# Performance work log

Measured on AMD Instinct MI355X. Metric: run time of the kernel, lower is better.

Reference implementation:

```python
import jax, jax.numpy as jnp
import numpy as np

DIM, H, KVH = 1024, 16, 4
HD = DIM // H            # head_dim = 64
KV_DIM = KVH * HD        # 256
ROPE_BASE = 10000.0
EPS = 1e-6


def setup_inputs() -> dict:
    key = jax.random.key(0)
    ks = jax.random.split(key, 6)
    B, S = 4, 2048
    x = jax.random.normal(ks[0], (B, S, DIM), dtype=jnp.float32)
    sc = 0.02
    Wq = jax.random.normal(ks[1], (DIM, DIM), dtype=jnp.float32) * sc
    Wk = jax.random.normal(ks[2], (KV_DIM, DIM), dtype=jnp.float32) * sc
    Wv = jax.random.normal(ks[3], (KV_DIM, DIM), dtype=jnp.float32) * sc
    Wo = jax.random.normal(ks[4], (DIM, DIM), dtype=jnp.float32) * sc
    q_gain = jnp.full((H,), 1.5, dtype=jnp.float32)
    return {"x": x, "Wq": Wq, "Wk": Wk, "Wv": Wv, "Wo": Wo, "q_gain": q_gain}


def _rms_norm(t):
    return t * jax.lax.rsqrt(jnp.mean(t * t, axis=-1, keepdims=True) + EPS)


def _rotary(seqlen, dtype):
    inv_freq = 1.0 / (ROPE_BASE ** (jnp.arange(0, HD, 2, dtype=jnp.float32) / HD))
    t = jnp.arange(seqlen, dtype=jnp.float32)
    freqs = jnp.outer(t, inv_freq)                      # [S, HD/2]
    return jnp.cos(freqs).astype(dtype)[None, None], jnp.sin(freqs).astype(dtype)[None, None]


def _apply_rot(t, cos, sin):
    half = t.shape[-1] // 2
    t1, t2 = t[..., :half], t[..., half:]
    return jnp.concatenate((t1 * cos + t2 * sin, -t1 * sin + t2 * cos), axis=-1)


def reference(x, Wq, Wk, Wv, Wo, q_gain):
    B, S, D = x.shape
    q = (x @ Wq.T).reshape(B, S, H, HD).transpose(0, 2, 1, 3)      # [B,H,S,HD]
    k = (x @ Wk.T).reshape(B, S, KVH, HD).transpose(0, 2, 1, 3)    # [B,KVH,S,HD]
    v = (x @ Wv.T).reshape(B, S, KVH, HD).transpose(0, 2, 1, 3)
    q, k = _rms_norm(q), _rms_norm(k)
    cos, sin = _rotary(S, q.dtype)
    q, k = _apply_rot(q, cos, sin), _apply_rot(k, cos, sin)
    q = q * q_gain.astype(q.dtype)[None, :, None, None]
    rep = H // KVH
    k_exp = jnp.repeat(k, rep, axis=1)                              # GQA expand
    v_exp = jnp.repeat(v, rep, axis=1)
    scores = jnp.einsum('bhqd,bhkd->bhqk', q, k_exp) / np.sqrt(HD)
    causal = jnp.tril(jnp.ones((S, S), dtype=bool))
    scores = jnp.where(causal[None, None], scores, jnp.finfo(scores.dtype).min)
    attn = jax.nn.softmax(scores, axis=-1)
    y = jnp.einsum('bhqk,bhkd->bhqd', attn, v_exp)
    y = y.transpose(0, 2, 1, 3).reshape(B, S, D)
    return y @ Wo.T
```

## Files before the change

### kernel.cpp

```cpp
#include <hip/hip_runtime.h>

typedef float f32x4 __attribute__((ext_vector_type(4)));
typedef float f32x16 __attribute__((ext_vector_type(16)));
typedef __bf16 bf16x8 __attribute__((ext_vector_type(8)));
typedef unsigned short u16x8 __attribute__((ext_vector_type(8)));
typedef int i32x2 __attribute__((ext_vector_type(2)));
typedef int i32x4 __attribute__((ext_vector_type(4)));

#define DEV static __device__ __forceinline__

DEV float bf2f(unsigned short h) {
  unsigned int u = ((unsigned int)h) << 16;
  return __builtin_bit_cast(float, u);
}
DEV unsigned short f2bf(float f) {
  unsigned int u = __builtin_bit_cast(unsigned int, f);
  u += 0x7fff + ((u >> 16) & 1);
  return (unsigned short)(u >> 16);
}

DEV void g2l16(const void* g, void* l) {
  __builtin_amdgcn_global_load_lds(
      (const __attribute__((address_space(1))) void*)g,
      (__attribute__((address_space(3))) void*)l, 16, 0, 0);
}

DEV unsigned int cvtpk(float lo, float hi) {
  unsigned int r;
  asm("v_cvt_pk_bf16_f32 %0, %1, %2" : "=v"(r) : "v"(lo), "v"(hi));
  return r;
}

DEV float fexp2(float x) {
  float r;
  asm("v_exp_f32 %0, %1" : "=v"(r) : "v"(x));
  return r;
}

DEV void cvt8(const float* __restrict__ in, unsigned short* __restrict__ out, int idx) {
  int i = idx * 8;
  float4 a = *(const float4*)(in + i);
  float4 b = *(const float4*)(in + i + 4);
  u16x8 r;
  r[0] = f2bf(a.x); r[1] = f2bf(a.y); r[2] = f2bf(a.z); r[3] = f2bf(a.w);
  r[4] = f2bf(b.x); r[5] = f2bf(b.y); r[6] = f2bf(b.z); r[7] = f2bf(b.w);
  *(u16x8*)(out + i) = r;
}

__global__ __launch_bounds__(256) void k_cvt_all(const float* __restrict__ x,
                                                 const float* __restrict__ wq,
                                                 const float* __restrict__ wk,
                                                 const float* __restrict__ wv,
                                                 const float* __restrict__ wo,
                                                 unsigned short* __restrict__ xb,
                                                 unsigned short* __restrict__ wcat,
                                                 unsigned short* __restrict__ wob,
                                                 float2* __restrict__ rope) {
  const int blk = blockIdx.x, tid = threadIdx.x;
  if (blk < 4096) {
    cvt8(x, xb, blk * 256 + tid);
  } else if (blk < 4608) {
    cvt8(wq, wcat, (blk - 4096) * 256 + tid);
  } else if (blk < 4736) {
    cvt8(wk, wcat + 1048576, (blk - 4608) * 256 + tid);
  } else if (blk < 4864) {
    cvt8(wv, wcat + 1310720, (blk - 4736) * 256 + tid);
  } else if (blk < 5376) {
    cvt8(wo, wob, (blk - 4864) * 256 + tid);
  } else {
    int idx = (blk - 5376) * 256 + tid;
    int s = idx >> 5, dmod = idx & 31;
    float inv_freq = powf(10000.0f, -(float)dmod * (1.0f / 32.0f));
    float sn, cs;
    sincosf((float)s * inv_freq, &sn, &cs);
    rope[idx] = make_float2(cs, sn);
  }
}

__global__ __launch_bounds__(256) void k_qkv(const unsigned short* __restrict__ A,
                                             const unsigned short* __restrict__ B,
                                             const float* __restrict__ qg,
                                             const float2* __restrict__ rope,
                                             unsigned short* __restrict__ qn,
                                             unsigned short* __restrict__ kn,
                                             unsigned short* __restrict__ vt) {
  __shared__ unsigned short LDS[16384];
  unsigned short* As = LDS;
  unsigned short* Bs = LDS + 8192;
  const int K = 1024;
  const int tid = threadIdx.x;
  const int wid = tid >> 6, lane = tid & 63;
  const int g = lane >> 4, r16 = lane & 15;
  const int m0 = blockIdx.x * 128;
  const int y = blockIdx.y;
  const int n0 = y * 128;
  const int wr = wid >> 1, wc = wid & 1;

  f32x4 acc[4][4];
#pragma unroll
  for (int i = 0; i < 4; ++i)
#pragma unroll
    for (int j = 0; j < 4; ++j) acc[i][j] = f32x4{0.f, 0.f, 0.f, 0.f};

  const int cb = (lane & 7) * 16;

  for (int k0 = 0; k0 < K; k0 += 64) {
#pragma unroll
    for (int c = 0; c < 4; ++c) {
      int i = wid * 4 + c;
      int row = i * 8 + (lane >> 3);
      int sc = cb ^ ((row & 7) << 4);
      g2l16((const char*)A + ((size_t)(m0 + row) * K + k0) * 2 + sc, (char*)As + i * 1024);
      g2l16((const char*)B + ((size_t)(n0 + row) * K + k0) * 2 + sc, (char*)Bs + i * 1024);
    }
    __syncthreads();
#pragma unroll
    for (int kh = 0; kh < 2; ++kh) {
      bf16x8 af[4], bfr[4];
#pragma unroll
      for (int m = 0; m < 4; ++m) {
        int row = wr * 64 + m * 16 + r16;
        int byte = row * 128 + ((g * 16 + kh * 64) ^ ((row & 7) << 4));
        af[m] = *(const bf16x8*)((const char*)As + byte);
      }
#pragma unroll
      for (int n = 0; n < 4; ++n) {
        int row = wc * 64 + n * 16 + r16;
        int byte = row * 128 + ((g * 16 + kh * 64) ^ ((row & 7) << 4));
        bfr[n] = *(const bf16x8*)((const char*)Bs + byte);
      }
#pragma unroll
      for (int m = 0; m < 4; ++m)
#pragma unroll
        for (int n = 0; n < 4; ++n)
          acc[m][n] = __builtin_amdgcn_mfma_f32_16x16x32_bf16(af[m], bfr[n], acc[m][n], 0, 0, 0);
    }
    __syncthreads();
  }

  if (y < 10) {
    const bool isq = (y < 8);
    const int head = isq ? (2 * y + wc) : (2 * (y - 8) + wc);
    const float gain = isq ? qg[head] * 0.18033688011112042f : 1.0f;
#pragma unroll
    for (int m = 0; m < 4; ++m)
#pragma unroll
      for (int j = 0; j < 4; ++j) {
        int rowl = wr * 64 + m * 16 + g * 4 + j;
        int tok = m0 + rowl;
        int s = tok & 2047;
        float v0 = acc[m][0][j], v1 = acc[m][1][j], v2 = acc[m][2][j], v3 = acc[m][3][j];
        float ss = v0 * v0 + v1 * v1 + v2 * v2 + v3 * v3;
        ss += __shfl_xor(ss, 1); ss += __shfl_xor(ss, 2);
        ss += __shfl_xor(ss, 4); ss += __shfl_xor(ss, 8);
        float rs = rsqrtf(ss * (1.0f / 64.0f) + 1e-6f) * gain;
        float2 cs0 = rope[s * 32 + r16];
        float2 cs1 = rope[s * 32 + 16 + r16];
        float o0 = (v0 * cs0.x + v2 * cs0.y) * rs;
        float o2 = (v2 * cs0.x - v0 * cs0.y) * rs;
        float o1 = (v1 * cs1.x + v3 * cs1.y) * rs;
        float o3 = (v3 * cs1.x - v1 * cs1.y) * rs;
        unsigned short* dst = isq ? (qn + (size_t)tok * 1024 + head * 64)
                                  : (kn + (size_t)tok * 256 + head * 64);
        dst[r16] = f2bf(o0);
        dst[16 + r16] = f2bf(o1);
        dst[32 + r16] = f2bf(o2);
        dst[48 + r16] = f2bf(o3);
      }
  } else {
    unsigned short* T = LDS;
#pragma unroll
    for (int m = 0; m < 4; ++m)
#pragma unroll
      for (int n = 0; n < 4; ++n)
#pragma unroll
        for (int j = 0; j < 4; ++j) {
          int tokl = wr * 64 + m * 16 + g * 4 + j;
          int dl = wc * 64 + n * 16 + r16;
          int byte = (dl * 256 + tokl * 2) ^ ((dl & 15) << 4);
          *(unsigned short*)((char*)T + byte) = f2bf(acc[m][n][j]);
        }
    __syncthreads();
    const int d = tid >> 1, th = tid & 1;
    const int hv = 2 * (y - 10) + (d >> 6), dh = d & 63;
    const int bb = m0 >> 11;
    const int s0 = (m0 & 2047) + th * 64;
    unsigned short* dstv = vt + ((size_t)(bb * 4 + hv) * 64 + dh) * 2048 + s0;
    const int swz = (d & 15) << 4;
#pragma unroll
    for (int c = 0; c < 8; ++c) {
      i32x4 w = *(const i32x4*)((const char*)T + ((d * 256 + th * 128 + c * 16) ^ swz));
      *(i32x4*)(dstv + c * 8) = w;
    }
  }
}

__global__ __launch_bounds__(256) void k_gemm_bt(const unsigned short* __restrict__ A,
                                                 const unsigned short* __restrict__ B,
                                                 float* __restrict__ C, int M, int N, int K) {
  __shared__ unsigned short As[128 * 64];
  __shared__ unsigned short Bs[128 * 64];
  const int tid = threadIdx.x;
  const int wid = tid >> 6, lane = tid & 63;
  const int g = lane >> 4, r16 = lane & 15;
  const int m0 = blockIdx.x * 128, n0 = blockIdx.y * 128;
  const int wr = wid >> 1, wc = wid & 1;

  f32x4 acc[4][4];
#pragma unroll
  for (int i = 0; i < 4; ++i)
#pragma unroll
    for (int j = 0; j < 4; ++j) acc[i][j] = f32x4{0.f, 0.f, 0.f, 0.f};

  const int cb = (lane & 7) * 16;

  for (int k0 = 0; k0 < K; k0 += 64) {
#pragma unroll
    for (int c = 0; c < 4; ++c) {
      int i = wid * 4 + c;
      int row = i * 8 + (lane >> 3);
      int sc = cb ^ ((row & 7) << 4);
      g2l16((const char*)A + ((size_t)(m0 + row) * K + k0) * 2 + sc, (char*)As + i * 1024);
      g2l16((const char*)B + ((size_t)(n0 + row) * K + k0) * 2 + sc, (char*)Bs + i * 1024);
    }
    __syncthreads();
#pragma unroll
    for (int kh = 0; kh < 2; ++kh) {
      bf16x8 af[4], bfr[4];
#pragma unroll
      for (int m = 0; m < 4; ++m) {
        int row = wr * 64 + m * 16 + r16;
        int byte = row * 128 + ((g * 16 + kh * 64) ^ ((row & 7) << 4));
        af[m] = *(const bf16x8*)((const char*)As + byte);
      }
#pragma unroll
      for (int n = 0; n < 4; ++n) {
        int row = wc * 64 + n * 16 + r16;
        int byte = row * 128 + ((g * 16 + kh * 64) ^ ((row & 7) << 4));
        bfr[n] = *(const bf16x8*)((const char*)Bs + byte);
      }
#pragma unroll
      for (int m = 0; m < 4; ++m)
#pragma unroll
        for (int n = 0; n < 4; ++n)
          acc[m][n] = __builtin_amdgcn_mfma_f32_16x16x32_bf16(af[m], bfr[n], acc[m][n], 0, 0, 0);
    }
    __syncthreads();
  }
#pragma unroll
  for (int m = 0; m < 4; ++m)
#pragma unroll
    for (int n = 0; n < 4; ++n)
#pragma unroll
      for (int j = 0; j < 4; ++j) {
        int row = m0 + wr * 64 + m * 16 + g * 4 + j;
        int col = n0 + wc * 64 + n * 16 + r16;
        C[(size_t)row * N + col] = acc[m][n][j];
      }
}

__global__ __launch_bounds__(512) void k_attn2(const unsigned short* __restrict__ qn,
                                               const unsigned short* __restrict__ kn,
                                               const unsigned short* __restrict__ vt,
                                               unsigned short* __restrict__ yb) {
  __shared__ unsigned short SMEM[4 * 8192];
  const int tid = threadIdx.x;
  const int wid = tid >> 6, lane = tid & 63;
  const int hi = lane >> 5, l31 = lane & 31;
  const int flat = blockIdx.x;
  const int qcx = 7 - (flat >> 6);
  const int bh = flat & 63;
  const int b = bh >> 4, h = bh & 15, hv = h >> 2;
  const int q0w = qcx * 256 + wid * 32;
  const int qglob = q0w + l31;
  const int tdiag = (q0w + 31) >> 6;
  const size_t tok0 = (size_t)b * 2048;
  const unsigned short* vtb = vt + (size_t)(b * 4 + hv) * 64 * 2048;

  const u16x8 onesu = {0x3F80, 0x3F80, 0x3F80, 0x3F80, 0x3F80, 0x3F80, 0x3F80, 0x3F80};
  const bf16x8 ones = __builtin_bit_cast(bf16x8, onesu);

  bf16x8 qf[4];
#pragma unroll
  for (int m = 0; m < 4; ++m)
    qf[m] = *(const bf16x8*)(qn + (tok0 + qglob) * 1024 + h * 64 + m * 16 + hi * 8);

  f32x16 oacc[2], lacc, zer;
#pragma unroll
  for (int r = 0; r < 16; ++r) { oacc[0][r] = 0.f; oacc[1][r] = 0.f; lacc[r] = 0.f; zer[r] = 0.f; }

  auto stage = [&](int T, int tb) {
    unsigned short* KsB = SMEM + tb * 8192;
    unsigned short* VtB = KsB + 4096;
    const int kk0 = T * 64;
    int row = wid * 8 + (lane >> 3);
    int sc = ((lane & 7) * 16) ^ ((row & 7) << 4);
    g2l16((const char*)(kn + (tok0 + kk0 + row) * 256 + hv * 64) + sc, (char*)KsB + wid * 1024);
    g2l16((const char*)(vtb + (size_t)row * 2048 + kk0) + sc, (char*)VtB + wid * 1024);
  };

  auto qk_tile = [&](int tb, f32x16* s) {
    const char* kbase0 = (const char*)SMEM + tb * 16384;
#pragma unroll
    for (int kt = 0; kt < 2; ++kt) {
      const int krow = kt * 32 + l31;
      const char* kbase = kbase0 + krow * 128;
      const int ksw = (krow & 7) << 4;
      __builtin_amdgcn_s_setprio(1);
      bf16x8 kf = *(const bf16x8*)(kbase + ((hi * 16) ^ ksw));
      f32x16 a = __builtin_amdgcn_mfma_f32_32x32x16_bf16(kf, qf[0], zer, 0, 0, 0);
#pragma unroll
      for (int m = 1; m < 4; ++m) {
        kf = *(const bf16x8*)(kbase + ((m * 32 + hi * 16) ^ ksw));
        a = __builtin_amdgcn_mfma_f32_32x32x16_bf16(kf, qf[m], a, 0, 0, 0);
      }
      __builtin_amdgcn_s_setprio(0);
      s[kt] = a;
    }
  };

  auto mask_tile = [&](int t, f32x16* s) {
    const int k0 = t * 64;
#pragma unroll
    for (int kt = 0; kt < 2; ++kt)
#pragma unroll
      for (int r = 0; r < 16; ++r) {
        int key = k0 + kt * 32 + (r & 3) + 8 * (r >> 2) + 4 * hi;
        if (key > qglob) s[kt][r] = -INFINITY;
      }
  };

  auto softmax_cvt = [&](f32x16* s, i32x4* paw) {
#pragma unroll
    for (int kt = 0; kt < 2; ++kt)
#pragma unroll
      for (int r = 0; r < 16; ++r) s[kt][r] = fexp2(s[kt][r]);
#pragma unroll
    for (int kt = 0; kt < 2; ++kt)
#pragma unroll
      for (int half = 0; half < 2; ++half) {
        int bs = half * 8;
        unsigned int a0 = cvtpk(s[kt][bs + 0], s[kt][bs + 1]);
        unsigned int a1 = cvtpk(s[kt][bs + 2], s[kt][bs + 3]);
        unsigned int b0 = cvtpk(s[kt][bs + 4], s[kt][bs + 5]);
        unsigned int b1 = cvtpk(s[kt][bs + 6], s[kt][bs + 7]);
        i32x2 r0 = __builtin_amdgcn_permlane32_swap((int)a0, (int)b0, false, false);
        i32x2 r1 = __builtin_amdgcn_permlane32_swap((int)a1, (int)b1, false, false);
        i32x4 w;
        w[0] = r0[0]; w[1] = r1[0]; w[2] = r0[1]; w[3] = r1[1];
        paw[kt * 2 + half] = w;
      }
  };

  auto pv_tile = [&](int tb, const i32x4* paw) {
    const char* vbase0 = (const char*)SMEM + tb * 16384 + 8192;
    __builtin_amdgcn_s_setprio(1);
#pragma unroll
    for (int db = 0; db < 2; ++db) {
      const int vrow = db * 32 + l31;
      const char* vbase = vbase0 + vrow * 128;
      const int vsw = (vrow & 7) << 4;
#pragma unroll
      for (int ks = 0; ks < 4; ++ks) {
        bf16x8 vf = *(const bf16x8*)(vbase + ((ks * 32 + hi * 16) ^ vsw));
        oacc[db] = __builtin_amdgcn_mfma_f32_32x32x16_bf16(
            vf, __builtin_bit_cast(bf16x8, paw[ks]), oacc[db], 0, 0, 0);
      }
    }
#pragma unroll
    for (int ks = 0; ks < 4; ++ks)
      lacc = __builtin_amdgcn_mfma_f32_32x32x16_bf16(
          ones, __builtin_bit_cast(bf16x8, paw[ks]), lacc, 0, 0, 0);
    __builtin_amdgcn_s_setprio(0);
  };

  const int npair = 2 * qcx + 2;

  stage(0, 0);
  stage(1, 1);
  __syncthreads();

  for (int p = 0; p < npair; ++p) {
    const int pb = (p & 1) << 1;
    if (p + 1 < npair) {
      stage(2 * p + 2, pb ^ 2);
      stage(2 * p + 3, (pb ^ 2) | 1);
    }
    const int t0 = 2 * p;
    const bool visa = (t0 <= tdiag), visb = (t0 + 1 <= tdiag);
    const bool domask = (p >= npair - 2);
    f32x16 sa[2], sb[2];
    if (visa) qk_tile(pb, sa);
    if (visb) qk_tile(pb | 1, sb);
    if (domask) {
      if (visa) mask_tile(t0, sa);
      if (visb) mask_tile(t0 + 1, sb);
    }
    i32x4 pawa[4], pawb[4];
    if (visa) {
      softmax_cvt(sa, pawa);
      pv_tile(pb, pawa);
    }
    if (visb) {
      softmax_cvt(sb, pawb);
      pv_tile(pb | 1, pawb);
    }
    __syncthreads();
  }

  const float inv = 1.0f / lacc[0];
  const int swl = (l31 & 7) << 4;
  char* obase = (char*)SMEM + wid * 4096;
#pragma unroll
  for (int db = 0; db < 2; ++db)
#pragma unroll
    for (int i = 0; i < 8; ++i) {
      int r = 2 * i;
      int dim = db * 32 + (r & 3) + 8 * (r >> 2) + 4 * hi;
      unsigned int w = (unsigned int)f2bf(oacc[db][r] * inv) |
                       ((unsigned int)f2bf(oacc[db][r + 1] * inv) << 16);
      *(unsigned int*)(obase + l31 * 128 + ((dim * 2) ^ swl)) = w;
    }
  __syncthreads();
#pragma unroll
  for (int it = 0; it < 4; ++it) {
    int cc = it * 2 + hi;
    i32x4 w = *(const i32x4*)(obase + l31 * 128 + ((cc * 16) ^ swl));
    *(i32x4*)(yb + (tok0 + q0w + l31) * 1024 + h * 64 + cc * 8) = w;
  }
}

extern "C" void kernel_launch(void* const* d_in, const int* in_sizes, int n_in,
                              void* d_out, int out_size, void* d_ws, size_t ws_size,
                              hipStream_t stream) {
  (void)in_sizes; (void)n_in; (void)out_size; (void)ws_size;
  const float* x  = (const float*)d_in[0];
  const float* Wq = (const float*)d_in[1];
  const float* Wk = (const float*)d_in[2];
  const float* Wv = (const float*)d_in[3];
  const float* Wo = (const float*)d_in[4];
  const float* qg = (const float*)d_in[5];

  char* ws = (char*)d_ws;
  unsigned short* xb   = (unsigned short*)(ws);
  unsigned short* wcat = (unsigned short*)(ws + 16777216);
  unsigned short* wob  = (unsigned short*)(ws + 19922944);
  unsigned short* qn   = (unsigned short*)(ws + 22020096);
  unsigned short* kn   = (unsigned short*)(ws + 38797312);
  unsigned short* yb   = xb;
  unsigned short* vt   = (unsigned short*)((char*)d_out + 25165824);
  float2*         rope = (float2*)((char*)d_out + 29360128);

  k_cvt_all<<<5632, 256, 0, stream>>>(x, Wq, Wk, Wv, Wo, xb, wcat, wob, rope);
  k_qkv<<<dim3(64, 12), 256, 0, stream>>>(xb, wcat, qg, rope, qn, kn, vt);
  k_attn2<<<512, 512, 0, stream>>>(qn, kn, vt, yb);
  k_gemm_bt<<<dim3(64, 8), 256, 0, stream>>>(yb, wob, (float*)d_out, 8192, 1024, 1024);
}
```

Before: 134.2 us.

## Store K and V in MFMA-fragment order so attention loads are contiguous

The QKV epilogue now writes K and transposed V into a blocked layout that matches the per-lane MFMA operand order, 512-element chunks per 64-key tile. The attention kernel can then stage each tile with plain contiguous 16-byte global-to-LDS copies and read fragments at lane*16 offsets with no swizzle arithmetic. This removes address computation and strided global reads, but the K stores in the QKV epilogue become scattered 2-byte writes, and unswizzled LDS reads may hit different bank patterns.

```diff
diff --git a/kernel.cpp b/kernel.cpp
--- a/kernel.cpp
+++ b/kernel.cpp
@@ -82,8 +82,8 @@
                                              const float* __restrict__ qg,
                                              const float2* __restrict__ rope,
                                              unsigned short* __restrict__ qn,
-                                             unsigned short* __restrict__ kn,
-                                             unsigned short* __restrict__ vt) {
+                                             unsigned short* __restrict__ kn2,
+                                             unsigned short* __restrict__ vt2) {
   __shared__ unsigned short LDS[16384];
   unsigned short* As = LDS;
   unsigned short* Bs = LDS + 8192;
@@ -160,12 +160,22 @@
         float o2 = (v2 * cs0.x - v0 * cs0.y) * rs;
         float o1 = (v1 * cs1.x + v3 * cs1.y) * rs;
         float o3 = (v3 * cs1.x - v1 * cs1.y) * rs;
-        unsigned short* dst = isq ? (qn + (size_t)tok * 1024 + head * 64)
-                                  : (kn + (size_t)tok * 256 + head * 64);
-        dst[r16] = f2bf(o0);
-        dst[16 + r16] = f2bf(o1);
-        dst[32 + r16] = f2bf(o2);
-        dst[48 + r16] = f2bf(o3);
+        if (isq) {
+          unsigned short* dst = qn + (size_t)tok * 1024 + head * 64;
+          dst[r16] = f2bf(o0);
+          dst[16 + r16] = f2bf(o1);
+          dst[32 + r16] = f2bf(o2);
+          dst[48 + r16] = f2bf(o3);
+        } else {
+          int b_ = tok >> 11;
+          int kb = s >> 5, kw = s & 31;
+          int hi8 = r16 >> 3, j7 = r16 & 7;
+          size_t kbase = ((size_t)((b_ * 4 + head) * 64 + kb) * 4) * 512 + (hi8 * 32 + kw) * 8 + j7;
+          kn2[kbase] = f2bf(o0);
+          kn2[kbase + 512] = f2bf(o1);
+          kn2[kbase + 1024] = f2bf(o2);
+          kn2[kbase + 1536] = f2bf(o3);
+        }
       }
   } else {
     unsigned short* T = LDS;
@@ -185,12 +195,14 @@
     const int hv = 2 * (y - 10) + (d >> 6), dh = d & 63;
     const int bb = m0 >> 11;
     const int s0 = (m0 & 2047) + th * 64;
-    unsigned short* dstv = vt + ((size_t)(bb * 4 + hv) * 64 + dh) * 2048 + s0;
+    const int kb64 = s0 >> 6;
+    const int db = dh >> 5, d31 = dh & 31;
+    const size_t vb0 = ((size_t)(bb * 4 + hv) * 32 + kb64) * 8 + db * 4;
     const int swz = (d & 15) << 4;
 #pragma unroll
     for (int c = 0; c < 8; ++c) {
       i32x4 w = *(const i32x4*)((const char*)T + ((d * 256 + th * 128 + c * 16) ^ swz));
-      *(i32x4*)(dstv + c * 8) = w;
+      *(i32x4*)(vt2 + (vb0 + (c >> 1)) * 512 + ((c & 1) * 32 + d31) * 8) = w;
     }
   }
 }
@@ -260,8 +272,8 @@
 }
 
 __global__ __launch_bounds__(512) void k_attn2(const unsigned short* __restrict__ qn,
-                                               const unsigned short* __restrict__ kn,
-                                               const unsigned short* __restrict__ vt,
+                                               const unsigned short* __restrict__ kn2,
+                                               const unsigned short* __restrict__ vt2,
                                                unsigned short* __restrict__ yb) {
   __shared__ unsigned short SMEM[4 * 8192];
   const int tid = threadIdx.x;
@@ -275,7 +287,6 @@
   const int qglob = q0w + l31;
   const int tdiag = (q0w + 31) >> 6;
   const size_t tok0 = (size_t)b * 2048;
-  const unsigned short* vtb = vt + (size_t)(b * 4 + hv) * 64 * 2048;
 
   const u16x8 onesu = {0x3F80, 0x3F80, 0x3F80, 0x3F80, 0x3F80, 0x3F80, 0x3F80, 0x3F80};
   const bf16x8 ones = __builtin_bit_cast(bf16x8, onesu);
@@ -289,29 +300,33 @@
 #pragma unroll
   for (int r = 0; r < 16; ++r) { oacc[0][r] = 0.f; oacc[1][r] = 0.f; lacc[r] = 0.f; zer[r] = 0.f; }
 
+  const int c0 = wid * 2;
+  const unsigned short* src0;
+  if (wid < 4) {
+    src0 = kn2 + (size_t)(b * 4 + hv) * 131072 + c0 * 512 + lane * 8;
+  } else {
+    src0 = vt2 + (size_t)(b * 4 + hv) * 131072 + (c0 - 8) * 512 + lane * 8;
+  }
+  const unsigned short* src1 = src0 + 512;
+
   auto stage = [&](int T, int tb) {
-    unsigned short* KsB = SMEM + tb * 8192;
-    unsigned short* VtB = KsB + 4096;
-    const int kk0 = T * 64;
-    int row = wid * 8 + (lane >> 3);
-    int sc = ((lane & 7) * 16) ^ ((row & 7) << 4);
-    g2l16((const char*)(kn + (tok0 + kk0 + row) * 256 + hv * 64) + sc, (char*)KsB + wid * 1024);
-    g2l16((const char*)(vtb + (size_t)row * 2048 + kk0) + sc, (char*)VtB + wid * 1024);
+    char* dst = (char*)SMEM + tb * 16384 + c0 * 1024;
+    g2l16(src0 + (size_t)T * 4096, dst);
+    g2l16(src1 + (size_t)T * 4096, dst + 1024);
   };
 
+  const char* lbase = (const char*)SMEM + lane * 16;
+
   auto qk_tile = [&](int tb, f32x16* s) {
-    const char* kbase0 = (const char*)SMEM + tb * 16384;
+    const char* base = lbase + tb * 16384;
 #pragma unroll
     for (int kt = 0; kt < 2; ++kt) {
-      const int krow = kt * 32 + l31;
-      const char* kbase = kbase0 + krow * 128;
-      const int ksw = (krow & 7) << 4;
       __builtin_amdgcn_s_setprio(1);
-      bf16x8 kf = *(const bf16x8*)(kbase + ((hi * 16) ^ ksw));
+      bf16x8 kf = *(const bf16x8*)(base + (kt * 4) * 1024);
       f32x16 a = __builtin_amdgcn_mfma_f32_32x32x16_bf16(kf, qf[0], zer, 0, 0, 0);
 #pragma unroll
       for (int m = 1; m < 4; ++m) {
-        kf = *(const bf16x8*)(kbase + ((m * 32 + hi * 16) ^ ksw));
+        kf = *(const bf16x8*)(base + (kt * 4 + m) * 1024);
         a = __builtin_amdgcn_mfma_f32_32x32x16_bf16(kf, qf[m], a, 0, 0, 0);
       }
       __builtin_amdgcn_s_setprio(0);
@@ -353,20 +368,16 @@
   };
 
   auto pv_tile = [&](int tb, const i32x4* paw) {
-    const char* vbase0 = (const char*)SMEM + tb * 16384 + 8192;
+    const char* base = lbase + tb * 16384 + 8192;
     __builtin_amdgcn_s_setprio(1);
 #pragma unroll
-    for (int db = 0; db < 2; ++db) {
-      const int vrow = db * 32 + l31;
-      const char* vbase = vbase0 + vrow * 128;
-      const int vsw = (vrow & 7) << 4;
+    for (int db = 0; db < 2; ++db)
 #pragma unroll
       for (int ks = 0; ks < 4; ++ks) {
-        bf16x8 vf = *(const bf16x8*)(vbase + ((ks * 32 + hi * 16) ^ vsw));
+        bf16x8 vf = *(const bf16x8*)(base + (db * 4 + ks) * 1024);
         oacc[db] = __builtin_amdgcn_mfma_f32_32x32x16_bf16(
             vf, __builtin_bit_cast(bf16x8, paw[ks]), oacc[db], 0, 0, 0);
       }
-    }
 #pragma unroll
     for (int ks = 0; ks < 4; ++ks)
       lacc = __builtin_amdgcn_mfma_f32_32x32x16_bf16(
@@ -446,13 +457,13 @@
   unsigned short* wcat = (unsigned short*)(ws + 16777216);
   unsigned short* wob  = (unsigned short*)(ws + 19922944);
   unsigned short* qn   = (unsigned short*)(ws + 22020096);
-  unsigned short* kn   = (unsigned short*)(ws + 38797312);
+  unsigned short* kn2  = (unsigned short*)(ws + 38797312);
   unsigned short* yb   = xb;
-  unsigned short* vt   = (unsigned short*)((char*)d_out + 25165824);
+  unsigned short* vt2  = (unsigned short*)((char*)d_out + 25165824);
   float2*         rope = (float2*)((char*)d_out + 29360128);
 
   k_cvt_all<<<5632, 256, 0, stream>>>(x, Wq, Wk, Wv, Wo, xb, wcat, wob, rope);
-  k_qkv<<<dim3(64, 12), 256, 0, stream>>>(xb, wcat, qg, rope, qn, kn, vt);
-  k_attn2<<<512, 512, 0, stream>>>(qn, kn, vt, yb);
+  k_qkv<<<dim3(64, 12), 256, 0, stream>>>(xb, wcat, qg, rope, qn, kn2, vt2);
+  k_attn2<<<512, 512, 0, stream>>>(qn, kn2, vt2, yb);
   k_gemm_bt<<<dim3(64, 8), 256, 0, stream>>>(yb, wob, (float*)d_out, 8192, 1024, 1024);
 }
```

After: 136.0 us. No clear change (+1.3%).
